# Performance work log

Hardware: AMD Instinct MI355X
Metric: run time of the kernel (lower is better)

The kernel has to match this reference:

```python
import jax, jax.numpy as jnp
import numpy as np


def _segsum(v, idx, n):
    return jax.ops.segment_sum(v, idx, num_segments=n)


def _rdl(z, n_dst, Wna, We, Wi, es, ed, is_, id_):
    """Relationship_Decoupled_layer: node softmax attn + per-edge attn.
    e-channel (mode etype): softmax over 2 logits; i-channel: sigmoid(1 logit)."""
    zd = z[:n_dst]
    node_alpha = jax.nn.softmax(zd @ Wna, axis=1)                      # [nd,2]
    e_e = jax.nn.softmax(jnp.concatenate([z[es], zd[ed]], axis=-1) @ We, axis=1)  # [Ee,2]
    e_i = jax.nn.sigmoid(jnp.concatenate([z[is_], zd[id_]], axis=-1) @ Wi)        # [Ei,1]
    return node_alpha, e_e, e_i


def _one_agg(z, n_dst, W, b, na, e_e, es, ed):
    """One_Neighbor_Aggregation: mean over nbrs of e[:,0]*Linear(z_src), relu, + alpha0*z_dst.
    Linear is applied on src nodes once (linearity) instead of per-edge."""
    zd = na[:, 0:1] * z[:n_dst]
    wz = z @ W + b                                                     # [n_src,D]
    s = _segsum(e_e[:, 0:1] * wz[es], ed, n_dst)                       # [nd,D]
    deg = _segsum(jnp.ones((es.shape[0], 1), z.dtype), ed, n_dst)
    f = jax.nn.relu(s / jnp.maximum(deg, 1.0))
    return f + zd


def _nia(z, n_dst, na, e_e, es, ed, e_i, is_, id_):
    """Neighbor_Interaction_Aggregation: e_h (mode etype, attn col 1) and i_h
    (other etype, sigmoid attn), cross term via polarization identity, + alpha1*z_dst."""
    zd = na[:, 1:2] * z[:n_dst]
    e_h = _segsum(e_e[:, 1:2] * z[es], ed, n_dst)
    i_h = _segsum(e_i * z[is_], id_, n_dst)
    inter = jax.nn.relu(0.5 * (jnp.square(e_h + i_h) - jnp.square(e_h) - jnp.square(i_h)))
    return inter + zd


def setup_inputs() -> dict:
    key = jax.random.key(0)
    ks = jax.random.split(key, 32)
    F, D, O = 256, 128, 64
    n_src0, n_dst0, E0 = 100000, 25000, 500000
    n_src1, n_dst1, E1 = 25000, 5000, 100000

    def ri(k, n, hi):
        return jax.random.randint(k, (n,), 0, hi, dtype=jnp.int32)

    inp = {
        'feat': jax.random.normal(ks[0], (n_src0, F), jnp.float32),
        'src0_cor': ri(ks[1], E0, n_src0), 'dst0_cor': ri(ks[2], E0, n_dst0),
        'src0_sim': ri(ks[3], E0, n_src0), 'dst0_sim': ri(ks[4], E0, n_dst0),
        'src1_cor': ri(ks[5], E1, n_src1), 'dst1_cor': ri(ks[6], E1, n_dst1),
        'src1_sim': ri(ks[7], E1, n_src1), 'dst1_sim': ri(ks[8], E1, n_dst1),
        'n_dst0': n_dst0, 'n_dst1': n_dst1,
    }
    s = 0.05  # keep attention logits / activations in a sane range
    inp['Win'] = jax.random.normal(ks[9], (2, F, D)) * s
    inp['b_in'] = jnp.zeros((2, D), jnp.float32)
    inp['na1'] = jax.random.normal(ks[10], (2, D, 2)) * s
    inp['ea1'] = jax.random.normal(ks[11], (2, 2 * D, 2)) * s
    inp['ia1'] = jax.random.normal(ks[12], (2, 2 * D, 1)) * s
    inp['W1'] = jax.random.normal(ks[13], (2, D, D)) * s
    inp['b1'] = jnp.zeros((2, D), jnp.float32)
    inp['na2'] = jax.random.normal(ks[14], (2, D, 2)) * s
    inp['ea2'] = jax.random.normal(ks[15], (2, 2 * D, 2)) * s
    inp['ia2'] = jax.random.normal(ks[16], (2, 2 * D, 1)) * s
    inp['W2'] = jax.random.normal(ks[17], (2, D, D)) * s
    inp['b2'] = jnp.zeros((2, D), jnp.float32)
    inp['Wout'] = jax.random.normal(ks[18], (2, D, O)) * s
    inp['bout'] = jnp.zeros((2, O), jnp.float32)
    return inp


def reference(feat, src0_cor, dst0_cor, src0_sim, dst0_sim,
              src1_cor, dst1_cor, src1_sim, dst1_sim, n_dst0, n_dst1,
              Win, b_in, na1, ea1, ia1, W1, b1, na2, ea2, ia2, W2, b2, Wout, bout):
    # mode index 0 = 'cor', 1 = 'sim'; e-channel = mode etype, i-channel = other etype
    blk0 = {0: (src0_cor, dst0_cor, src0_sim, dst0_sim),
            1: (src0_sim, dst0_sim, src0_cor, dst0_cor)}
    blk1 = {0: (src1_cor, dst1_cor, src1_sim, dst1_sim),
            1: (src1_sim, dst1_sim, src1_cor, dst1_cor)}
    outs = []
    for m in range(2):
        es0, ed0, is0, id0 = blk0[m]
        es1, ed1, is1, id1 = blk1[m]
        z = feat @ Win[m] + b_in[m]                                    # fc_input (eval: dropout = identity)
        # layer 1 on block0
        na, ee, ei = _rdl(z, n_dst0, na1[m], ea1[m], ia1[m], es0, ed0, is0, id0)
        one = _one_agg(z, n_dst0, W1[m], b1[m], na, ee, es0, ed0)
        nia = _nia(z, n_dst0, na, ee, es0, ed0, ei, is0, id0)
        z = 0.5 * (one + nia)                                          # [n_dst0, D]
        # layer 2 on block1
        na, ee, ei = _rdl(z, n_dst1, na2[m], ea2[m], ia2[m], es1, ed1, is1, id1)
        one = _one_agg(z, n_dst1, W2[m], b2[m], na, ee, es1, ed1)
        nia = _nia(z, n_dst1, na, ee, es1, ed1, ei, is1, id1)
        z = 0.5 * (one + nia)                                          # [n_dst1, D]
        outs.append(z @ Wout[m] + bout[m])
    return jnp.stack(outs)                                             # [2, n_dst1, O] (cor, sim)
```

## Files before the change

kernel.cpp:

```cpp
#include <hip/hip_runtime.h>
#include <hip/hip_bf16.h>
#include <math.h>

#define F_DIM 256
#define D_DIM 128
#define O_DIM 64
#define NS0   100000
#define ND0   25000
#define E0_N  500000
#define NS1   25000
#define ND1   5000
#define E1_N  100000

#define NBE0  1954
#define NBE1  391

typedef __attribute__((ext_vector_type(8))) short s8v;
typedef __attribute__((ext_vector_type(4))) float f4v;

struct CPtr4 { const int *p0, *p1, *p2, *p3; };
struct MPtr4 { int *p0, *p1, *p2, *p3; };

__device__ __forceinline__ float2 unpack2(uint u) {
    union { uint i; float f; } a, b;
    a.i = (u & 0xffffu) << 16; b.i = u & 0xffff0000u;
    return make_float2(a.f, b.f);
}
__device__ __forceinline__ ushort f2bf(float f) {
    __hip_bfloat16 h = __float2bfloat16(f);
    return *(ushort*)&h;
}
__device__ __forceinline__ float u2f(uint u) {
    union { uint i; float f; } v; v.i = u; return v.f;
}
__device__ __forceinline__ uint f2u(float f) {
    union { uint i; float f; } v; v.f = f; return v.i;
}

__global__ void prep_weights(
    const float* __restrict__ Win, const float* __restrict__ W1,
    const float* __restrict__ W2,  const float* __restrict__ Wout,
    ushort* __restrict__ Wtin, ushort* __restrict__ Wt1,
    ushort* __restrict__ Wt2,  ushort* __restrict__ Wtout)
{
    int i = blockIdx.x * 256 + threadIdx.x;
    if (i < 65536) {
        int m = i >> 15, r = i & 32767, k = r >> 7, n = r & 127;
        Wtin[m * 32768 + n * 256 + k] = f2bf(Win[m * 32768 + k * 128 + n]);
    } else if (i < 98304) {
        int i2 = i - 65536;
        int m = i2 >> 14, r = i2 & 16383, k = r >> 7, n = r & 127;
        Wt1[m * 16384 + n * 128 + k] = f2bf(W1[m * 16384 + k * 128 + n]);
    } else if (i < 131072) {
        int i2 = i - 98304;
        int m = i2 >> 14, r = i2 & 16383, k = r >> 7, n = r & 127;
        Wt2[m * 16384 + n * 128 + k] = f2bf(W2[m * 16384 + k * 128 + n]);
    } else if (i < 147456) {
        int i2 = i - 131072;
        int m = i2 >> 13, r = i2 & 8191, k = r >> 6, n = r & 63;
        Wtout[m * 8192 + n * 128 + k] = f2bf(Wout[m * 8192 + k * 64 + n]);
    }
}

template<int NW, int KD, int EPI, bool AF32>
__global__ __launch_bounds__(256) void mfma_gemm(
    const void* __restrict__ Ab, size_t astr,
    const ushort* __restrict__ Btb, size_t btstr,
    const float* __restrict__ biasb, size_t bstr,
    const float* __restrict__ cvecb, size_t cvstr,
    const float* __restrict__ partialb, size_t pstr,
    void* __restrict__ Coutb, size_t coutstr, int M)
{
    const int m = blockIdx.y;
    const ushort* A16 = AF32 ? nullptr : ((const ushort*)Ab + m * astr);
    const float*  A32 = AF32 ? ((const float*)Ab + m * astr) : nullptr;
    const ushort* Bt = Btb + m * btstr;
    const float* bias = biasb + m * bstr;
    const float* cvec = (EPI == 2) ? cvecb + m * cvstr : nullptr;
    const float* partial = (EPI == 2) ? partialb + m * pstr : nullptr;
    char* Cout = (char*)Coutb + m * coutstr * (EPI == 1 ? 4 : 2);

    constexpr int PA = 40;
    constexpr int WAVES_M = (NW == 128) ? 2 : 4;
    constexpr int WM = 128 / WAVES_M;
    constexpr int TM = WM / 16;
    constexpr int TN = 4;
    __shared__ ushort As[128 * PA];
    __shared__ ushort Bs[NW * PA];

    const int tid  = threadIdx.x;
    const int row0 = blockIdx.x * 128;
    const int wave = tid >> 6, lane = tid & 63;
    const int l15 = lane & 15, l4 = lane >> 4;
    int wm0, wn0;
    if (NW == 128) { wm0 = (wave >> 1) * 64; wn0 = (wave & 1) * 64; }
    else           { wm0 = wave * WM;        wn0 = 0; }

    f4v acc[TM][TN];
    #pragma unroll
    for (int i = 0; i < TM; ++i)
        #pragma unroll
        for (int j = 0; j < TN; ++j)
            acc[i][j] = (f4v)(0.0f);

    for (int kc = 0; kc < KD; kc += 32) {
        __syncthreads();
        #pragma unroll
        for (int it = 0; it < 2; ++it) {
            int f = tid + it * 256;
            int r = f >> 2, g = (f & 3) * 8;
            int gr = row0 + r;
            if (AF32) {
                float4 v0 = make_float4(0.f, 0.f, 0.f, 0.f);
                float4 v1 = make_float4(0.f, 0.f, 0.f, 0.f);
                if (gr < M) {
                    v0 = *(const float4*)(A32 + (size_t)gr * KD + kc + g);
                    v1 = *(const float4*)(A32 + (size_t)gr * KD + kc + g + 4);
                }
                ushort4 o0, o1;
                o0.x = f2bf(v0.x); o0.y = f2bf(v0.y); o0.z = f2bf(v0.z); o0.w = f2bf(v0.w);
                o1.x = f2bf(v1.x); o1.y = f2bf(v1.y); o1.z = f2bf(v1.z); o1.w = f2bf(v1.w);
                *(ushort4*)(&As[r * PA + g]) = o0;
                *(ushort4*)(&As[r * PA + g + 4]) = o1;
            } else {
                float4 v = make_float4(0.f, 0.f, 0.f, 0.f);
                if (gr < M) v = *(const float4*)(A16 + (size_t)gr * KD + kc + g);
                *(float4*)(&As[r * PA + g]) = v;
            }
        }
        #pragma unroll
        for (int it = 0; it < NW * 32 / (256 * 8); ++it) {
            int f = tid + it * 256;
            int r = f >> 2, g = (f & 3) * 8;
            *(float4*)(&Bs[r * PA + g]) = *(const float4*)(Bt + (size_t)r * KD + kc + g);
        }
        __syncthreads();

        s8v af[TM], bfr[TN];
        #pragma unroll
        for (int i = 0; i < TM; ++i)
            af[i] = *(const s8v*)(&As[(wm0 + i * 16 + l15) * PA + l4 * 8]);
        #pragma unroll
        for (int j = 0; j < TN; ++j)
            bfr[j] = *(const s8v*)(&Bs[(wn0 + j * 16 + l15) * PA + l4 * 8]);
        #pragma unroll
        for (int i = 0; i < TM; ++i)
            #pragma unroll
            for (int j = 0; j < TN; ++j)
                acc[i][j] = __builtin_amdgcn_mfma_f32_16x16x32_bf16(
                    af[i], bfr[j], acc[i][j], 0, 0, 0);
    }

    #pragma unroll
    for (int i = 0; i < TM; ++i) {
        #pragma unroll
        for (int ii = 0; ii < 4; ++ii) {
            int row = row0 + wm0 + i * 16 + l4 * 4 + ii;
            if (row < M) {
                #pragma unroll
                for (int j = 0; j < TN; ++j) {
                    int col = wn0 + j * 16 + l15;
                    float a = acc[i][j][ii];
                    if (EPI == 0) {
                        ((ushort*)Cout)[(size_t)row * NW + col] = f2bf(a + bias[col]);
                    } else if (EPI == 1) {
                        ((float*)Cout)[(size_t)row * NW + col] = a + bias[col];
                    } else {
                        float val = a + cvec[row] * bias[col];
                        float o = partial[(size_t)row * NW + col] + 0.5f * fmaxf(val, 0.f);
                        ((ushort*)Cout)[(size_t)row * NW + col] = f2bf(o);
                    }
                }
            }
        }
    }
}

__global__ void histo4(CPtr4 ed, MPtr4 cnt)
{
    int b = blockIdx.x, t = threadIdx.x;
    const int* edp; int* cp; int e, E;
    if (b < NBE0)          { edp = ed.p0; cp = cnt.p0; e = b * 256 + t;              E = E0_N; }
    else if (b < 2 * NBE0) { edp = ed.p1; cp = cnt.p1; e = (b - NBE0) * 256 + t;     E = E0_N; }
    else if (b < 2 * NBE0 + NBE1)
                           { edp = ed.p2; cp = cnt.p2; e = (b - 2 * NBE0) * 256 + t; E = E1_N; }
    else                   { edp = ed.p3; cp = cnt.p3; e = (b - 2 * NBE0 - NBE1) * 256 + t; E = E1_N; }
    if (e < E) atomicAdd(&cp[edp[e]], 1);
}

__global__ __launch_bounds__(1024) void exscan4(MPtr4 cnt, MPtr4 row, MPtr4 head)
{
    __shared__ int part[1024];
    const int b = blockIdx.x, t = threadIdx.x;
    int* cp; int* rp; int* hp; int n;
    if (b == 0)      { cp = cnt.p0; rp = row.p0; hp = head.p0; n = ND0; }
    else if (b == 1) { cp = cnt.p1; rp = row.p1; hp = head.p1; n = ND0; }
    else if (b == 2) { cp = cnt.p2; rp = row.p2; hp = head.p2; n = ND1; }
    else             { cp = cnt.p3; rp = row.p3; hp = head.p3; n = ND1; }

    const int chunk = (n + 1023) >> 10;
    const int start = t * chunk;
    int s = 0;
    for (int i = 0; i < chunk; ++i) {
        int idx = start + i;
        if (idx < n) s += cp[idx];
    }
    part[t] = s;
    __syncthreads();
    for (int off = 1; off < 1024; off <<= 1) {
        int v = (t >= off) ? part[t - off] : 0;
        __syncthreads();
        part[t] += v;
        __syncthreads();
    }
    int run = (t == 0) ? 0 : part[t - 1];
    for (int i = 0; i < chunk; ++i) {
        int idx = start + i;
        if (idx < n) { rp[idx] = run; hp[idx] = run; run += cp[idx]; }
    }
    if (t == 1023) rp[n] = part[1023];
}

__global__ void build4(CPtr4 es, CPtr4 ed, MPtr4 head, MPtr4 src)
{
    int b = blockIdx.x, t = threadIdx.x;
    const int *esp, *edp; int *hp, *sp; int e, E;
    if (b < NBE0)          { esp = es.p0; edp = ed.p0; hp = head.p0; sp = src.p0; e = b * 256 + t;              E = E0_N; }
    else if (b < 2 * NBE0) { esp = es.p1; edp = ed.p1; hp = head.p1; sp = src.p1; e = (b - NBE0) * 256 + t;     E = E0_N; }
    else if (b < 2 * NBE0 + NBE1)
                           { esp = es.p2; edp = ed.p2; hp = head.p2; sp = src.p2; e = (b - 2 * NBE0) * 256 + t; E = E1_N; }
    else                   { esp = es.p3; edp = ed.p3; hp = head.p3; sp = src.p3; e = (b - 2 * NBE0 - NBE1) * 256 + t; E = E1_N; }
    if (e >= E) return;
    int p = atomicAdd(&hp[edp[e]], 1);
    sp[p] = esp[e];
}

#define NP_NPB 128
__global__ __launch_bounds__(256) void node_proj(
    const ushort* __restrict__ zb, size_t zstr,
    const float* __restrict__ Web,
    const float* __restrict__ Wib,
    float* __restrict__ psb, float* __restrict__ qsb,
    float* __restrict__ pdb, float* __restrict__ qdb,
    int n_src, int n_dst)
{
    const int m = blockIdx.y;
    const ushort* z = zb + m * zstr;
    const float* We = Web + m * 512;
    const float* Wi = Wib + m * 256;
    float* ps = psb + (size_t)m * NS0 * 2;
    float* qs = qsb + (size_t)m * NS0;
    float* pd = pdb + (size_t)m * ND0 * 2;
    float* qd = qdb + (size_t)m * ND0;

    __shared__ float w[6][D_DIM];
    for (int k = threadIdx.x; k < D_DIM; k += 256) {
        w[0][k] = We[k * 2 + 0];
        w[1][k] = We[k * 2 + 1];
        w[2][k] = Wi[k];
        w[3][k] = We[(D_DIM + k) * 2 + 0];
        w[4][k] = We[(D_DIM + k) * 2 + 1];
        w[5][k] = Wi[D_DIM + k];
    }
    __syncthreads();

    const int sub = threadIdx.x & 7;
    const int g   = threadIdx.x >> 3;

    float wr[6][16];
    #pragma unroll
    for (int c = 0; c < 6; ++c)
        #pragma unroll
        for (int q = 0; q < 4; ++q) {
            float4 f = *(const float4*)(&w[c][sub * 16 + q * 4]);
            wr[c][q * 4 + 0] = f.x; wr[c][q * 4 + 1] = f.y;
            wr[c][q * 4 + 2] = f.z; wr[c][q * 4 + 3] = f.w;
        }

    #pragma unroll
    for (int it = 0; it < 4; ++it) {
        int node = blockIdx.x * NP_NPB + it * 32 + g;
        if (node >= n_src) continue;
        const ushort* zp = z + (size_t)node * D_DIM + sub * 16;
        uint4 ra = *(const uint4*)zp;
        uint4 rb = *(const uint4*)(zp + 8);
        uint rr[8] = {ra.x, ra.y, ra.z, ra.w, rb.x, rb.y, rb.z, rb.w};
        float p[6] = {0.f, 0.f, 0.f, 0.f, 0.f, 0.f};
        #pragma unroll
        for (int e = 0; e < 8; ++e) {
            float2 f2 = unpack2(rr[e]);
            #pragma unroll
            for (int c = 0; c < 6; ++c)
                p[c] += f2.x * wr[c][2 * e] + f2.y * wr[c][2 * e + 1];
        }
        #pragma unroll
        for (int off = 4; off > 0; off >>= 1)
            #pragma unroll
            for (int c = 0; c < 6; ++c)
                p[c] += __shfl_down(p[c], off);

        if (sub == 0) {
            *(float2*)(ps + (size_t)node * 2) = make_float2(p[0], p[1]);
            qs[node] = p[2];
            if (node < n_dst) {
                *(float2*)(pd + (size_t)node * 2) = make_float2(p[3], p[4]);
                qd[node] = p[5];
            }
        }
    }
}

__global__ __launch_bounds__(256) void edge_att(
    const float* __restrict__ psb, const float* __restrict__ pdb,
    const float* __restrict__ qsb, const float* __restrict__ qdb,
    const int* __restrict__ row_c, const int* __restrict__ src_c,
    const int* __restrict__ row_s, const int* __restrict__ src_s,
    uint2* __restrict__ epkb, uint2* __restrict__ ipkb,
    float* __restrict__ cvecb, int n_dst)
{
    const int m = blockIdx.y;
    const int d = blockIdx.x * 4 + (threadIdx.x >> 6);
    const int lane = threadIdx.x & 63;
    if (d >= n_dst) return;

    const float* ps = psb + (size_t)m * NS0 * 2;
    const float* qs = qsb + (size_t)m * NS0;
    const float* pdv = pdb + (size_t)m * ND0 * 2;
    const float* qdv = qdb + (size_t)m * ND0;
    const int* erow = m ? row_s : row_c;
    const int* esrc = m ? src_s : src_c;
    const int* irow = m ? row_c : row_s;
    const int* isrc = m ? src_c : src_s;
    uint2* epk = epkb + (size_t)m * E0_N;
    uint2* ipk = ipkb + (size_t)m * E0_N;
    float* cvec = cvecb + (size_t)m * ND0;

    const float pd0 = pdv[2 * d], pd1 = pdv[2 * d + 1];
    const float qdd = qdv[d];

    const int b0 = erow[d], b1 = erow[d + 1];
    float se0 = 0.f;
    for (int j = b0 + lane; j < b1; j += 64) {
        int s = esrc[j];
        float2 pp = *(const float2*)(ps + 2 * (size_t)s);
        float l0 = pp.x + pd0, l1 = pp.y + pd1;
        float mx = fmaxf(l0, l1);
        float x0 = __expf(l0 - mx), x1 = __expf(l1 - mx);
        float e0 = x0 / (x0 + x1);
        epk[j] = make_uint2(f2u(e0), (uint)s);
        se0 += e0;
    }
    #pragma unroll
    for (int off = 32; off > 0; off >>= 1)
        se0 += __shfl_down(se0, off);
    if (lane == 0) cvec[d] = se0 / fmaxf((float)(b1 - b0), 1.0f);

    const int c0 = irow[d], c1 = irow[d + 1];
    for (int j = c0 + lane; j < c1; j += 64) {
        int s = isrc[j];
        float q = qs[s] + qdd;
        float sg = 1.0f / (1.0f + __expf(-q));
        ipk[j] = make_uint2(f2u(sg), (uint)s);
    }
}

__global__ __launch_bounds__(256) void gather_acc(
    const ushort* __restrict__ zb, size_t zstr,
    const uint2* __restrict__ epkb, const uint2* __restrict__ ipkb,
    const int* __restrict__ row_c, const int* __restrict__ row_s,
    ushort* __restrict__ h0base, float* __restrict__ partialb, int n_dst)
{
    const int m = blockIdx.y;
    const int d = blockIdx.x * 4 + (threadIdx.x >> 6);
    const int lane = threadIdx.x & 63;
    if (d >= n_dst) return;

    const ushort* z = zb + m * zstr;
    const uint2* epk = epkb + (size_t)m * E0_N;
    const uint2* ipk = ipkb + (size_t)m * E0_N;
    const int* erow = m ? row_s : row_c;
    const int* irow = m ? row_c : row_s;
    ushort* h0b = h0base + (size_t)m * ND0 * D_DIM;
    float* partial = partialb + (size_t)m * ND0 * D_DIM;

    float h0x = 0.f, h0y = 0.f, szx = 0.f, szy = 0.f;
    float ihx = 0.f, ihy = 0.f;

    const int b0 = erow[d], b1 = erow[d + 1];
    int j = b0;
    for (; j + 8 <= b1; j += 8) {
        uint2 ew[8]; uint rr[8];
        #pragma unroll
        for (int k = 0; k < 8; ++k) ew[k] = epk[j + k];
        #pragma unroll
        for (int k = 0; k < 8; ++k) rr[k] = *(const uint*)(z + (size_t)ew[k].y * D_DIM + lane * 2);
        #pragma unroll
        for (int k = 0; k < 8; ++k) {
            float w0 = u2f(ew[k].x);
            float2 v = unpack2(rr[k]);
            szx += v.x; szy += v.y;
            h0x += w0 * v.x; h0y += w0 * v.y;
        }
    }
    for (; j < b1; ++j) {
        uint2 ew = epk[j];
        float w0 = u2f(ew.x);
        float2 v = unpack2(*(const uint*)(z + (size_t)ew.y * D_DIM + lane * 2));
        szx += v.x; szy += v.y;
        h0x += w0 * v.x; h0y += w0 * v.y;
    }

    const int c0 = irow[d], c1 = irow[d + 1];
    j = c0;
    for (; j + 8 <= c1; j += 8) {
        uint2 ew[8]; uint rr[8];
        #pragma unroll
        for (int k = 0; k < 8; ++k) ew[k] = ipk[j + k];
        #pragma unroll
        for (int k = 0; k < 8; ++k) rr[k] = *(const uint*)(z + (size_t)ew[k].y * D_DIM + lane * 2);
        #pragma unroll
        for (int k = 0; k < 8; ++k) {
            float g = u2f(ew[k].x);
            float2 v = unpack2(rr[k]);
            ihx += g * v.x; ihy += g * v.y;
        }
    }
    for (; j < c1; ++j) {
        uint2 ew = ipk[j];
        float g = u2f(ew.x);
        float2 v = unpack2(*(const uint*)(z + (size_t)ew.y * D_DIM + lane * 2));
        ihx += g * v.x; ihy += g * v.y;
    }

    float ehx = szx - h0x, ehy = szy - h0y;
    float inv = 1.0f / fmaxf((float)(b1 - b0), 1.0f);
    uint hp = (uint)f2bf(h0x * inv) | ((uint)f2bf(h0y * inv) << 16);
    *(uint*)(h0b + (size_t)d * D_DIM + lane * 2) = hp;

    float2 zd = unpack2(*(const uint*)(z + (size_t)d * D_DIM + lane * 2));
    float px = 0.5f * (fmaxf(ehx * ihx, 0.f) + zd.x);
    float py = 0.5f * (fmaxf(ehy * ihy, 0.f) + zd.y);
    *(float2*)(partial + (size_t)d * D_DIM + lane * 2) = make_float2(px, py);
}

extern "C" void kernel_launch(void* const* d_in, const int* in_sizes, int n_in,
                              void* d_out, int out_size, void* d_ws, size_t ws_size,
                              hipStream_t stream)
{
    const float* feat = (const float*)d_in[0];
    const int* src0_cor = (const int*)d_in[1];
    const int* dst0_cor = (const int*)d_in[2];
    const int* src0_sim = (const int*)d_in[3];
    const int* dst0_sim = (const int*)d_in[4];
    const int* src1_cor = (const int*)d_in[5];
    const int* dst1_cor = (const int*)d_in[6];
    const int* src1_sim = (const int*)d_in[7];
    const int* dst1_sim = (const int*)d_in[8];
    const float* Win  = (const float*)d_in[11];
    const float* b_in = (const float*)d_in[12];
    const float* ea1  = (const float*)d_in[14];
    const float* ia1  = (const float*)d_in[15];
    const float* W1   = (const float*)d_in[16];
    const float* b1   = (const float*)d_in[17];
    const float* ea2  = (const float*)d_in[19];
    const float* ia2  = (const float*)d_in[20];
    const float* W2   = (const float*)d_in[21];
    const float* b2   = (const float*)d_in[22];
    const float* Wout = (const float*)d_in[23];
    const float* bout = (const float*)d_in[24];
    (void)in_sizes; (void)n_in; (void)out_size; (void)ws_size;

    char* wsb = (char*)d_ws;
    size_t off = 0;
    auto alloc_f = [&](size_t n) { float*  p = (float*) (wsb + off); off += n * 4; return p; };
    auto alloc_i = [&](size_t n) { int*    p = (int*)   (wsb + off); off += n * 4; return p; };
    auto alloc_h = [&](size_t n) { ushort* p = (ushort*)(wsb + off); off += ((n * 2 + 15) & ~15ull); return p; };
    auto alloc_u2 = [&](size_t n) { uint2* p = (uint2*)(wsb + off); off += n * 8; return p; };

    ushort* z0b   = alloc_h((size_t)2 * NS0 * D_DIM);
    ushort* z1b   = alloc_h((size_t)2 * NS1 * D_DIM);
    ushort* z2b   = alloc_h((size_t)2 * ND1 * D_DIM);
    ushort* h0b   = alloc_h((size_t)2 * ND0 * D_DIM);
    ushort* Wtin  = alloc_h((size_t)2 * D_DIM * F_DIM);
    ushort* Wt1   = alloc_h((size_t)2 * D_DIM * D_DIM);
    ushort* Wt2   = alloc_h((size_t)2 * D_DIM * D_DIM);
    ushort* Wtout = alloc_h((size_t)2 * O_DIM * D_DIM);

    float* ps      = alloc_f((size_t)2 * NS0 * 2);
    float* qs      = alloc_f((size_t)2 * NS0);
    float* pd      = alloc_f((size_t)2 * ND0 * 2);
    float* qd      = alloc_f((size_t)2 * ND0);
    float* cvec    = alloc_f((size_t)2 * ND0);
    float* partial = alloc_f((size_t)2 * ND0 * D_DIM);
    uint2* epk     = alloc_u2((size_t)2 * E0_N);
    uint2* ipk     = alloc_u2((size_t)2 * E0_N);

    int* src_c0 = alloc_i(E0_N); int* row_c0 = alloc_i(ND0 + 1);
    int* src_s0 = alloc_i(E0_N); int* row_s0 = alloc_i(ND0 + 1);
    int* src_c1 = alloc_i(E1_N); int* row_c1 = alloc_i(ND1 + 1);
    int* src_s1 = alloc_i(E1_N); int* row_s1 = alloc_i(ND1 + 1);
    int* cnt_all  = alloc_i(2 * ND0 + 2 * ND1);
    int* head_all = alloc_i(2 * ND0 + 2 * ND1);

    int* cnt_c0 = cnt_all;            int* head_c0 = head_all;
    int* cnt_s0 = cnt_all + ND0;      int* head_s0 = head_all + ND0;
    int* cnt_c1 = cnt_all + 2 * ND0;  int* head_c1 = head_all + 2 * ND0;
    int* cnt_s1 = cnt_c1 + ND1;       int* head_s1 = head_c1 + ND1;

    const int NB_ALL = 2 * NBE0 + 2 * NBE1;
    hipMemsetAsync(cnt_all, 0, (size_t)(2 * ND0 + 2 * ND1) * 4, stream);
    {
        CPtr4 edp  = {dst0_cor, dst0_sim, dst1_cor, dst1_sim};
        CPtr4 esp  = {src0_cor, src0_sim, src1_cor, src1_sim};
        MPtr4 cntp = {cnt_c0, cnt_s0, cnt_c1, cnt_s1};
        MPtr4 rowp = {row_c0, row_s0, row_c1, row_s1};
        MPtr4 hdp  = {head_c0, head_s0, head_c1, head_s1};
        MPtr4 srcp = {src_c0, src_s0, src_c1, src_s1};
        histo4<<<NB_ALL, 256, 0, stream>>>(edp, cntp);
        exscan4<<<4, 1024, 0, stream>>>(cntp, rowp, hdp);
        build4<<<NB_ALL, 256, 0, stream>>>(esp, edp, hdp, srcp);
    }

    prep_weights<<<576, 256, 0, stream>>>(Win, W1, W2, Wout, Wtin, Wt1, Wt2, Wtout);

    const size_t Z0S = (size_t)NS0 * D_DIM, Z1S = (size_t)NS1 * D_DIM;
    const size_t Z2S = (size_t)ND1 * D_DIM, H0S = (size_t)ND0 * D_DIM;

    mfma_gemm<128, 256, 0, true><<<dim3((NS0 + 127) / 128, 2), 256, 0, stream>>>(
        feat, 0, Wtin, (size_t)D_DIM * F_DIM, b_in, D_DIM,
        nullptr, 0, nullptr, 0, z0b, Z0S, NS0);

    node_proj<<<dim3((NS0 + NP_NPB - 1) / NP_NPB, 2), 256, 0, stream>>>(
        z0b, Z0S, ea1, ia1, ps, qs, pd, qd, NS0, ND0);
    edge_att<<<dim3((ND0 + 3) / 4, 2), 256, 0, stream>>>(
        ps, pd, qs, qd, row_c0, src_c0, row_s0, src_s0, epk, ipk, cvec, ND0);
    gather_acc<<<dim3((ND0 + 3) / 4, 2), 256, 0, stream>>>(
        z0b, Z0S, epk, ipk, row_c0, row_s0, h0b, partial, ND0);
    mfma_gemm<128, 128, 2, false><<<dim3((ND0 + 127) / 128, 2), 256, 0, stream>>>(
        h0b, H0S, Wt1, (size_t)D_DIM * D_DIM, b1, D_DIM,
        cvec, ND0, partial, H0S, z1b, Z1S, ND0);

    node_proj<<<dim3((NS1 + NP_NPB - 1) / NP_NPB, 2), 256, 0, stream>>>(
        z1b, Z1S, ea2, ia2, ps, qs, pd, qd, NS1, ND1);
    edge_att<<<dim3((ND1 + 3) / 4, 2), 256, 0, stream>>>(
        ps, pd, qs, qd, row_c1, src_c1, row_s1, src_s1, epk, ipk, cvec, ND1);
    gather_acc<<<dim3((ND1 + 3) / 4, 2), 256, 0, stream>>>(
        z1b, Z1S, epk, ipk, row_c1, row_s1, h0b, partial, ND1);
    mfma_gemm<128, 128, 2, false><<<dim3((ND1 + 127) / 128, 2), 256, 0, stream>>>(
        h0b, H0S, Wt2, (size_t)D_DIM * D_DIM, b2, D_DIM,
        cvec, ND0, partial, H0S, z2b, Z2S, ND1);

    mfma_gemm<64, 128, 1, false><<<dim3((ND1 + 127) / 128, 2), 256, 0, stream>>>(
        z2b, Z2S, Wtout, (size_t)O_DIM * D_DIM, bout, O_DIM,
        nullptr, 0, nullptr, 0, (float*)d_out, (size_t)ND1 * O_DIM, ND1);
}
```

Before: 588.5 us.

## Share feat tile across both modes in input GEMM, fuse weight prep into histogram

The input projection now has each block load and convert one 64-row fp32 feat tile once and multiply it by both modes' weight matrices. Previously the feat matrix was read and converted twice, once per mode. Weight transposition is folded into the histogram launch to save a kernel launch. The gather tails are made branchless with an 8-wide masked batch, with the edge buffers padded so the extra loads stay in bounds. The cost is higher register and LDS use per block in the new GEMM.

```diff
diff --git a/kernel.cpp b/kernel.cpp
--- a/kernel.cpp
+++ b/kernel.cpp
@@ -14,6 +14,8 @@
 
 #define NBE0  1954
 #define NBE1  391
+#define NB_CSR (2 * NBE0 + 2 * NBE1)
+#define NB_WPREP 576
 
 typedef __attribute__((ext_vector_type(8))) short s8v;
 typedef __attribute__((ext_vector_type(4))) float f4v;
@@ -37,34 +39,100 @@
     union { uint i; float f; } v; v.f = f; return v.i;
 }
 
-__global__ void prep_weights(
-    const float* __restrict__ Win, const float* __restrict__ W1,
-    const float* __restrict__ W2,  const float* __restrict__ Wout,
-    ushort* __restrict__ Wtin, ushort* __restrict__ Wt1,
-    ushort* __restrict__ Wt2,  ushort* __restrict__ Wtout)
-{
-    int i = blockIdx.x * 256 + threadIdx.x;
-    if (i < 65536) {
-        int m = i >> 15, r = i & 32767, k = r >> 7, n = r & 127;
-        Wtin[m * 32768 + n * 256 + k] = f2bf(Win[m * 32768 + k * 128 + n]);
-    } else if (i < 98304) {
-        int i2 = i - 65536;
-        int m = i2 >> 14, r = i2 & 16383, k = r >> 7, n = r & 127;
-        Wt1[m * 16384 + n * 128 + k] = f2bf(W1[m * 16384 + k * 128 + n]);
-    } else if (i < 131072) {
-        int i2 = i - 98304;
-        int m = i2 >> 14, r = i2 & 16383, k = r >> 7, n = r & 127;
-        Wt2[m * 16384 + n * 128 + k] = f2bf(W2[m * 16384 + k * 128 + n]);
-    } else if (i < 147456) {
-        int i2 = i - 131072;
-        int m = i2 >> 13, r = i2 & 8191, k = r >> 6, n = r & 63;
-        Wtout[m * 8192 + n * 128 + k] = f2bf(Wout[m * 8192 + k * 64 + n]);
-    }
-}
-
-template<int NW, int KD, int EPI, bool AF32>
+__global__ __launch_bounds__(256) void gemm_l0(
+    const float* __restrict__ A,
+    const ushort* __restrict__ Btb,
+    const float* __restrict__ biasb,
+    ushort* __restrict__ Coutb, size_t coutstr, int M)
+{
+    constexpr int PA = 40;
+    __shared__ ushort As[64 * PA];
+    __shared__ ushort Bs[2][128 * PA];
+
+    const int tid = threadIdx.x;
+    const int row0 = blockIdx.x * 64;
+    const int wave = tid >> 6, lane = tid & 63;
+    const int l15 = lane & 15, l4 = lane >> 4;
+    const int wm0 = (wave >> 1) * 32;
+    const int wn0 = (wave & 1) * 64;
+
+    f4v acc[2][2][4];
+    #pragma unroll
+    for (int m2 = 0; m2 < 2; ++m2)
+        #pragma unroll
+        for (int i = 0; i < 2; ++i)
+            #pragma unroll
+            for (int j = 0; j < 4; ++j)
+                acc[m2][i][j] = (f4v)(0.0f);
+
+    for (int kc = 0; kc < F_DIM; kc += 32) {
+        __syncthreads();
+        {
+            int r = tid >> 2, g = (tid & 3) * 8;
+            int gr = row0 + r;
+            float4 v0 = make_float4(0.f, 0.f, 0.f, 0.f);
+            float4 v1 = make_float4(0.f, 0.f, 0.f, 0.f);
+            if (gr < M) {
+                v0 = *(const float4*)(A + (size_t)gr * F_DIM + kc + g);
+                v1 = *(const float4*)(A + (size_t)gr * F_DIM + kc + g + 4);
+            }
+            ushort4 o0, o1;
+            o0.x = f2bf(v0.x); o0.y = f2bf(v0.y); o0.z = f2bf(v0.z); o0.w = f2bf(v0.w);
+            o1.x = f2bf(v1.x); o1.y = f2bf(v1.y); o1.z = f2bf(v1.z); o1.w = f2bf(v1.w);
+            *(ushort4*)(&As[r * PA + g]) = o0;
+            *(ushort4*)(&As[r * PA + g + 4]) = o1;
+        }
+        #pragma unroll
+        for (int m2 = 0; m2 < 2; ++m2)
+            #pragma unroll
+            for (int it = 0; it < 2; ++it) {
+                int f = tid + it * 256;
+                int r = f >> 2, g = (f & 3) * 8;
+                *(float4*)(&Bs[m2][r * PA + g]) =
+                    *(const float4*)(Btb + m2 * (D_DIM * F_DIM) + (size_t)r * F_DIM + kc + g);
+            }
+        __syncthreads();
+
+        s8v af[2];
+        #pragma unroll
+        for (int i = 0; i < 2; ++i)
+            af[i] = *(const s8v*)(&As[(wm0 + i * 16 + l15) * PA + l4 * 8]);
+        #pragma unroll
+        for (int m2 = 0; m2 < 2; ++m2) {
+            s8v bfr[4];
+            #pragma unroll
+            for (int j = 0; j < 4; ++j)
+                bfr[j] = *(const s8v*)(&Bs[m2][(wn0 + j * 16 + l15) * PA + l4 * 8]);
+            #pragma unroll
+            for (int i = 0; i < 2; ++i)
+                #pragma unroll
+                for (int j = 0; j < 4; ++j)
+                    acc[m2][i][j] = __builtin_amdgcn_mfma_f32_16x16x32_bf16(
+                        af[i], bfr[j], acc[m2][i][j], 0, 0, 0);
+        }
+    }
+
+    #pragma unroll
+    for (int m2 = 0; m2 < 2; ++m2)
+        #pragma unroll
+        for (int i = 0; i < 2; ++i)
+            #pragma unroll
+            for (int ii = 0; ii < 4; ++ii) {
+                int row = row0 + wm0 + i * 16 + l4 * 4 + ii;
+                if (row < M) {
+                    #pragma unroll
+                    for (int j = 0; j < 4; ++j) {
+                        int col = wn0 + j * 16 + l15;
+                        Coutb[m2 * coutstr + (size_t)row * D_DIM + col] =
+                            f2bf(acc[m2][i][j][ii] + biasb[m2 * D_DIM + col]);
+                    }
+                }
+            }
+}
+
+template<int NW, int KD, int EPI>
 __global__ __launch_bounds__(256) void mfma_gemm(
-    const void* __restrict__ Ab, size_t astr,
+    const ushort* __restrict__ Ab, size_t astr,
     const ushort* __restrict__ Btb, size_t btstr,
     const float* __restrict__ biasb, size_t bstr,
     const float* __restrict__ cvecb, size_t cvstr,
@@ -72,8 +140,7 @@
     void* __restrict__ Coutb, size_t coutstr, int M)
 {
     const int m = blockIdx.y;
-    const ushort* A16 = AF32 ? nullptr : ((const ushort*)Ab + m * astr);
-    const float*  A32 = AF32 ? ((const float*)Ab + m * astr) : nullptr;
+    const ushort* A = Ab + m * astr;
     const ushort* Bt = Btb + m * btstr;
     const float* bias = biasb + m * bstr;
     const float* cvec = (EPI == 2) ? cvecb + m * cvstr : nullptr;
@@ -110,23 +177,9 @@
             int f = tid + it * 256;
             int r = f >> 2, g = (f & 3) * 8;
             int gr = row0 + r;
-            if (AF32) {
-                float4 v0 = make_float4(0.f, 0.f, 0.f, 0.f);
-                float4 v1 = make_float4(0.f, 0.f, 0.f, 0.f);
-                if (gr < M) {
-                    v0 = *(const float4*)(A32 + (size_t)gr * KD + kc + g);
-                    v1 = *(const float4*)(A32 + (size_t)gr * KD + kc + g + 4);
-                }
-                ushort4 o0, o1;
-                o0.x = f2bf(v0.x); o0.y = f2bf(v0.y); o0.z = f2bf(v0.z); o0.w = f2bf(v0.w);
-                o1.x = f2bf(v1.x); o1.y = f2bf(v1.y); o1.z = f2bf(v1.z); o1.w = f2bf(v1.w);
-                *(ushort4*)(&As[r * PA + g]) = o0;
-                *(ushort4*)(&As[r * PA + g + 4]) = o1;
-            } else {
-                float4 v = make_float4(0.f, 0.f, 0.f, 0.f);
-                if (gr < M) v = *(const float4*)(A16 + (size_t)gr * KD + kc + g);
-                *(float4*)(&As[r * PA + g]) = v;
-            }
+            float4 v = make_float4(0.f, 0.f, 0.f, 0.f);
+            if (gr < M) v = *(const float4*)(A + (size_t)gr * KD + kc + g);
+            *(float4*)(&As[r * PA + g]) = v;
         }
         #pragma unroll
         for (int it = 0; it < NW * 32 / (256 * 8); ++it) {
@@ -161,9 +214,7 @@
                 for (int j = 0; j < TN; ++j) {
                     int col = wn0 + j * 16 + l15;
                     float a = acc[i][j][ii];
-                    if (EPI == 0) {
-                        ((ushort*)Cout)[(size_t)row * NW + col] = f2bf(a + bias[col]);
-                    } else if (EPI == 1) {
+                    if (EPI == 1) {
                         ((float*)Cout)[(size_t)row * NW + col] = a + bias[col];
                     } else {
                         float val = a + cvec[row] * bias[col];
@@ -176,9 +227,33 @@
     }
 }
 
-__global__ void histo4(CPtr4 ed, MPtr4 cnt)
+__global__ void histo4_prep(CPtr4 ed, MPtr4 cnt,
+    const float* __restrict__ Win, const float* __restrict__ W1,
+    const float* __restrict__ W2,  const float* __restrict__ Wout,
+    ushort* __restrict__ Wtin, ushort* __restrict__ Wt1,
+    ushort* __restrict__ Wt2,  ushort* __restrict__ Wtout)
 {
     int b = blockIdx.x, t = threadIdx.x;
+    if (b >= NB_CSR) {
+        int i = (b - NB_CSR) * 256 + t;
+        if (i < 65536) {
+            int m = i >> 15, r = i & 32767, k = r >> 7, n = r & 127;
+            Wtin[m * 32768 + n * 256 + k] = f2bf(Win[m * 32768 + k * 128 + n]);
+        } else if (i < 98304) {
+            int i2 = i - 65536;
+            int m = i2 >> 14, r = i2 & 16383, k = r >> 7, n = r & 127;
+            Wt1[m * 16384 + n * 128 + k] = f2bf(W1[m * 16384 + k * 128 + n]);
+        } else if (i < 131072) {
+            int i2 = i - 98304;
+            int m = i2 >> 14, r = i2 & 16383, k = r >> 7, n = r & 127;
+            Wt2[m * 16384 + n * 128 + k] = f2bf(W2[m * 16384 + k * 128 + n]);
+        } else if (i < 147456) {
+            int i2 = i - 131072;
+            int m = i2 >> 13, r = i2 & 8191, k = r >> 6, n = r & 63;
+            Wtout[m * 8192 + n * 128 + k] = f2bf(Wout[m * 8192 + k * 64 + n]);
+        }
+        return;
+    }
     const int* edp; int* cp; int e, E;
     if (b < NBE0)          { edp = ed.p0; cp = cnt.p0; e = b * 256 + t;              E = E0_N; }
     else if (b < 2 * NBE0) { edp = ed.p1; cp = cnt.p1; e = (b - NBE0) * 256 + t;     E = E0_N; }
@@ -238,8 +313,7 @@
 #define NP_NPB 128
 __global__ __launch_bounds__(256) void node_proj(
     const ushort* __restrict__ zb, size_t zstr,
-    const float* __restrict__ Web,
-    const float* __restrict__ Wib,
+    const float* __restrict__ Web, const float* __restrict__ Wib,
     float* __restrict__ psb, float* __restrict__ qsb,
     float* __restrict__ pdb, float* __restrict__ qdb,
     int n_src, int n_dst)
@@ -388,7 +462,8 @@
 
     const int b0 = erow[d], b1 = erow[d + 1];
     int j = b0;
-    for (; j + 8 <= b1; j += 8) {
+    const int jfull = b0 + ((b1 - b0) & ~7);
+    for (; j < jfull; j += 8) {
         uint2 ew[8]; uint rr[8];
         #pragma unroll
         for (int k = 0; k < 8; ++k) ew[k] = epk[j + k];
@@ -402,17 +477,29 @@
             h0x += w0 * v.x; h0y += w0 * v.y;
         }
     }
-    for (; j < b1; ++j) {
-        uint2 ew = epk[j];
-        float w0 = u2f(ew.x);
-        float2 v = unpack2(*(const uint*)(z + (size_t)ew.y * D_DIM + lane * 2));
-        szx += v.x; szy += v.y;
-        h0x += w0 * v.x; h0y += w0 * v.y;
+    if (j < b1) {
+        uint2 ew[8]; uint rr[8];
+        #pragma unroll
+        for (int k = 0; k < 8; ++k) ew[k] = epk[j + k];
+        #pragma unroll
+        for (int k = 0; k < 8; ++k) {
+            uint s = (j + k < b1) ? ew[k].y : 0u;
+            rr[k] = *(const uint*)(z + (size_t)s * D_DIM + lane * 2);
+        }
+        #pragma unroll
+        for (int k = 0; k < 8; ++k) {
+            float sel = (j + k < b1) ? 1.0f : 0.0f;
+            float w0 = u2f(ew[k].x) * sel;
+            float2 v = unpack2(rr[k]);
+            szx += v.x * sel; szy += v.y * sel;
+            h0x += w0 * v.x; h0y += w0 * v.y;
+        }
     }
 
     const int c0 = irow[d], c1 = irow[d + 1];
     j = c0;
-    for (; j + 8 <= c1; j += 8) {
+    const int cfull = c0 + ((c1 - c0) & ~7);
+    for (; j < cfull; j += 8) {
         uint2 ew[8]; uint rr[8];
         #pragma unroll
         for (int k = 0; k < 8; ++k) ew[k] = ipk[j + k];
@@ -425,11 +512,22 @@
             ihx += g * v.x; ihy += g * v.y;
         }
     }
-    for (; j < c1; ++j) {
-        uint2 ew = ipk[j];
-        float g = u2f(ew.x);
-        float2 v = unpack2(*(const uint*)(z + (size_t)ew.y * D_DIM + lane * 2));
-        ihx += g * v.x; ihy += g * v.y;
+    if (j < c1) {
+        uint2 ew[8]; uint rr[8];
+        #pragma unroll
+        for (int k = 0; k < 8; ++k) ew[k] = ipk[j + k];
+        #pragma unroll
+        for (int k = 0; k < 8; ++k) {
+            uint s = (j + k < c1) ? ew[k].y : 0u;
+            rr[k] = *(const uint*)(z + (size_t)s * D_DIM + lane * 2);
+        }
+        #pragma unroll
+        for (int k = 0; k < 8; ++k) {
+            float sel = (j + k < c1) ? 1.0f : 0.0f;
+            float g = u2f(ew[k].x) * sel;
+            float2 v = unpack2(rr[k]);
+            ihx += g * v.x; ihy += g * v.y;
+        }
     }
 
     float ehx = szx - h0x, ehy = szy - h0y;
@@ -492,8 +590,8 @@
     float* qd      = alloc_f((size_t)2 * ND0);
     float* cvec    = alloc_f((size_t)2 * ND0);
     float* partial = alloc_f((size_t)2 * ND0 * D_DIM);
-    uint2* epk     = alloc_u2((size_t)2 * E0_N);
-    uint2* ipk     = alloc_u2((size_t)2 * E0_N);
+    uint2* epk     = alloc_u2((size_t)2 * E0_N + 8);
+    uint2* ipk     = alloc_u2((size_t)2 * E0_N + 8);
 
     int* src_c0 = alloc_i(E0_N); int* row_c0 = alloc_i(ND0 + 1);
     int* src_s0 = alloc_i(E0_N); int* row_s0 = alloc_i(ND0 + 1);
@@ -507,7 +605,6 @@
     int* cnt_c1 = cnt_all + 2 * ND0;  int* head_c1 = head_all + 2 * ND0;
     int* cnt_s1 = cnt_c1 + ND1;       int* head_s1 = head_c1 + ND1;
 
-    const int NB_ALL = 2 * NBE0 + 2 * NBE1;
     hipMemsetAsync(cnt_all, 0, (size_t)(2 * ND0 + 2 * ND1) * 4, stream);
     {
         CPtr4 edp  = {dst0_cor, dst0_sim, dst1_cor, dst1_sim};
@@ -516,19 +613,17 @@
         MPtr4 rowp = {row_c0, row_s0, row_c1, row_s1};
         MPtr4 hdp  = {head_c0, head_s0, head_c1, head_s1};
         MPtr4 srcp = {src_c0, src_s0, src_c1, src_s1};
-        histo4<<<NB_ALL, 256, 0, stream>>>(edp, cntp);
+        histo4_prep<<<NB_CSR + NB_WPREP, 256, 0, stream>>>(
+            edp, cntp, Win, W1, W2, Wout, Wtin, Wt1, Wt2, Wtout);
         exscan4<<<4, 1024, 0, stream>>>(cntp, rowp, hdp);
-        build4<<<NB_ALL, 256, 0, stream>>>(esp, edp, hdp, srcp);
-    }
-
-    prep_weights<<<576, 256, 0, stream>>>(Win, W1, W2, Wout, Wtin, Wt1, Wt2, Wtout);
+        build4<<<NB_CSR, 256, 0, stream>>>(esp, edp, hdp, srcp);
+    }
 
     const size_t Z0S = (size_t)NS0 * D_DIM, Z1S = (size_t)NS1 * D_DIM;
     const size_t Z2S = (size_t)ND1 * D_DIM, H0S = (size_t)ND0 * D_DIM;
 
-    mfma_gemm<128, 256, 0, true><<<dim3((NS0 + 127) / 128, 2), 256, 0, stream>>>(
-        feat, 0, Wtin, (size_t)D_DIM * F_DIM, b_in, D_DIM,
-        nullptr, 0, nullptr, 0, z0b, Z0S, NS0);
+    gemm_l0<<<(NS0 + 63) / 64, 256, 0, stream>>>(
+        feat, Wtin, b_in, z0b, Z0S, NS0);
 
     node_proj<<<dim3((NS0 + NP_NPB - 1) / NP_NPB, 2), 256, 0, stream>>>(
         z0b, Z0S, ea1, ia1, ps, qs, pd, qd, NS0, ND0);
@@ -536,7 +631,7 @@
         ps, pd, qs, qd, row_c0, src_c0, row_s0, src_s0, epk, ipk, cvec, ND0);
     gather_acc<<<dim3((ND0 + 3) / 4, 2), 256, 0, stream>>>(
         z0b, Z0S, epk, ipk, row_c0, row_s0, h0b, partial, ND0);
-    mfma_gemm<128, 128, 2, false><<<dim3((ND0 + 127) / 128, 2), 256, 0, stream>>>(
+    mfma_gemm<128, 128, 2><<<dim3((ND0 + 127) / 128, 2), 256, 0, stream>>>(
         h0b, H0S, Wt1, (size_t)D_DIM * D_DIM, b1, D_DIM,
         cvec, ND0, partial, H0S, z1b, Z1S, ND0);
 
@@ -546,11 +641,11 @@
         ps, pd, qs, qd, row_c1, src_c1, row_s1, src_s1, epk, ipk, cvec, ND1);
     gather_acc<<<dim3((ND1 + 3) / 4, 2), 256, 0, stream>>>(
         z1b, Z1S, epk, ipk, row_c1, row_s1, h0b, partial, ND1);
-    mfma_gemm<128, 128, 2, false><<<dim3((ND1 + 127) / 128, 2), 256, 0, stream>>>(
+    mfma_gemm<128, 128, 2><<<dim3((ND1 + 127) / 128, 2), 256, 0, stream>>>(
         h0b, H0S, Wt2, (size_t)D_DIM * D_DIM, b2, D_DIM,
         cvec, ND0, partial, H0S, z2b, Z2S, ND1);
 
-    mfma_gemm<64, 128, 1, false><<<dim3((ND1 + 127) / 128, 2), 256, 0, stream>>>(
+    mfma_gemm<64, 128, 1><<<dim3((ND1 + 127) / 128, 2), 256, 0, stream>>>(
         z2b, Z2S, Wtout, (size_t)O_DIM * D_DIM, bout, O_DIM,
         nullptr, 0, nullptr, 0, (float*)d_out, (size_t)ND1 * O_DIM, ND1);
 }
```

Result: faster. 553.6 us (-5.9%).
